# Performance work log

Hardware: AMD Instinct MI355X
Metric: run time of the kernel (lower is better)

Reference implementation:

```python
import jax, jax.numpy as jnp
import numpy as np

N_QUBITS = 10
N_LAYERS = 4
OUTPUT = 16
BATCH = 4096
DIM = 2 ** N_QUBITS  # 1024, amplitude-embedding dimension


def setup_inputs() -> dict:
    key = jax.random.key(0)
    k1, k2, k3, k4 = jax.random.split(key, 4)
    X = jax.random.normal(k1, (BATCH, DIM), jnp.float32)
    weights = jax.random.normal(k2, (N_LAYERS, N_QUBITS, 3), jnp.float32)  # StronglyEntanglingLayers params
    W = jax.random.normal(k3, (OUTPUT, N_QUBITS), jnp.float32) / np.sqrt(N_QUBITS)
    b = jax.random.normal(k4, (OUTPUT,), jnp.float32) * 0.01
    return {"X": X, "weights": weights, "W": W, "b": b}


def _rot_matrix(phi, theta, omega):
    # PennyLane Rot(phi, theta, omega) = RZ(omega) @ RY(theta) @ RZ(phi)
    c = jnp.cos(theta / 2).astype(jnp.complex64)
    s = jnp.sin(theta / 2).astype(jnp.complex64)
    a = jnp.exp(-0.5j * (phi + omega)) * c
    bq = -jnp.exp(0.5j * (phi - omega)) * s
    cq = jnp.exp(-0.5j * (phi - omega)) * s
    d = jnp.exp(0.5j * (phi + omega)) * c
    return jnp.stack([jnp.stack([a, bq]), jnp.stack([cq, d])])  # (2,2) complex64


def _apply_1q(state, U, q, n):
    # wire 0 is the most-significant bit (PennyLane default.qubit convention)
    A, B = 2 ** q, 2 ** (n - q - 1)
    s = state.reshape(-1, A, 2, B)
    s = jnp.einsum('ij,bajc->baic', U, s)
    return s.reshape(-1, 2 ** n)


def _cnot(state, c, t, n):
    hi, lo = (c, t) if c < t else (t, c)
    s = state.reshape(-1, 2 ** hi, 2, 2 ** (lo - hi - 1), 2, 2 ** (n - lo - 1))
    if c < t:
        # control axis 2, target axis 4
        s0 = s[:, :, 0]                      # (B, H, M, 2, L)
        s1 = jnp.flip(s[:, :, 1], axis=3)    # flip target where control=1
        s = jnp.stack([s0, s1], axis=2)
    else:
        # control axis 4, target axis 2
        s0 = s[:, :, :, :, 0, :]             # (B, H, 2, M, L)
        s1 = jnp.flip(s[:, :, :, :, 1, :], axis=2)
        s = jnp.stack([s0, s1], axis=4)
    return s.reshape(-1, 2 ** n)


def _circuit(X, weights):
    n = N_QUBITS
    # AmplitudeEmbedding (pad_with=0.0; here input dim == 2**n so just normalize)
    nrm = jnp.linalg.norm(X, axis=-1, keepdims=True)
    state = (X / nrm).astype(jnp.complex64)  # (B, 2**n)
    for l in range(N_LAYERS):
        for q in range(n):
            U = _rot_matrix(weights[l, q, 0], weights[l, q, 1], weights[l, q, 2])
            state = _apply_1q(state, U, q, n)
        r = (l % (n - 1)) + 1  # StronglyEntanglingLayers default imprimitive range
        for q in range(n):
            state = _cnot(state, q, (q + r) % n, n)
    probs = state.real ** 2 + state.imag ** 2  # (B, 2**n)
    # <Z_i> = sum_s probs[s] * (1 - 2*bit_i(s)); wire 0 = MSB
    idx = np.arange(2 ** n)
    bits = (idx[:, None] >> np.arange(n - 1, -1, -1)[None, :]) & 1  # (2**n, n)
    signs = jnp.asarray(1 - 2 * bits, jnp.float32)
    return probs @ signs  # (B, n)


def reference(X, weights, W, b):
    z = _circuit(X, weights)          # (B, n_qubits)
    return z @ W.T + b                # Linear head; nn.Tanh is defined but unused in forward
```

## Files before the change

kernel.cpp:

```cpp
#include <hip/hip_runtime.h>
#include <stdint.h>

#define NQ 10
#define DIMQ 1024
#define BATCH 4096

typedef float f32x2 __attribute__((ext_vector_type(2)));

#if __has_builtin(__builtin_amdgcn_permlane16_swap)
#define HAS_PL16 1
#else
#define HAS_PL16 0
#endif

__host__ __device__ constexpr int cperm_c(int x, int r) {
  for (int q = 0; q < NQ; ++q) {
    const int c = 9 - q;
    int t = c - r; if (t < 0) t += NQ;
    x ^= ((x >> c) & 1) << t;
  }
  return x;
}
constexpr int amask(int q) {
  int a = 0;
  for (int b = 0; b < 6; ++b) a |= ((cperm_c(1 << b, 4) >> (9 - q)) & 1) << b;
  return a;
}
constexpr int mmask(int q) {
  int m = 0;
  for (int b = 0; b < 4; ++b) m |= ((cperm_c(1 << (6 + b), 4) >> (9 - q)) & 1) << b;
  return m;
}

__global__ __launch_bounds__(256) void prep_g(const float* __restrict__ wts,
                                              float* __restrict__ Gg) {
  const int idx = blockIdx.x * 256 + threadIdx.x;
  if (idx < 40) {
    float th = wts[idx * 3 + 1];
    ((float2*)Gg)[idx] = make_float2(cosf(0.5f * th), sinf(0.5f * th));
  }
  f32x2* D0 = (f32x2*)(Gg + 128);
  float4* E = (float4*)(D0 + 1024);
  auto sphase = [&](int l, int i, int comp) {
    float s = 0.f;
    #pragma unroll
    for (int q = 0; q < 10; ++q) {
      float sg = ((i >> (9 - q)) & 1) ? 0.5f : -0.5f;
      s += sg * wts[(l * 10 + q) * 3 + comp];
    }
    return s;
  };
  float p0 = sphase(0, idx, 0);
  D0[idx] = (f32x2){cosf(p0), sinf(p0)};
  #pragma unroll
  for (int l = 0; l < 3; ++l) {
    float a = sphase(l, idx, 2) + sphase(l + 1, cperm_c(idx, l + 1), 0);
    E[l * 1024 + idx] = make_float4(cosf(a), cosf(a), -sinf(a), sinf(a));
  }
}

template<int CTRL>
__device__ __forceinline__ float dpp1(float x) {
  return __int_as_float(
      __builtin_amdgcn_update_dpp(0, __float_as_int(x), CTRL, 0xF, 0xF, true));
}
template<int P>
__device__ __forceinline__ float shufl(float x) {
  if constexpr (P == 0)      return dpp1<0xB1>(x);
  else if constexpr (P == 1) return dpp1<0x4E>(x);
  else if constexpr (P == 2) return dpp1<0x141>(dpp1<0x1B>(x));
  else                       return dpp1<0x128>(x);
}

__device__ __forceinline__ f32x2 swapv(f32x2 v) {
  return __builtin_shufflevector(v, v, 1, 0);
}

__device__ __forceinline__ float red64(float v) {
  v += dpp1<0xB1>(v);
  v += dpp1<0x4E>(v);
  v += dpp1<0x141>(dpp1<0x1B>(v));
  v += dpp1<0x128>(v);
#if HAS_PL16
  { auto rr = __builtin_amdgcn_permlane16_swap(__float_as_uint(v),
                                               __float_as_uint(v), false, false);
    v = __uint_as_float(rr[0]) + __uint_as_float(rr[1]); }
#else
  v += __int_as_float(__builtin_amdgcn_ds_swizzle(__float_as_int(v), 0x401F));
#endif
  auto p = __builtin_amdgcn_permlane32_swap(__float_as_uint(v),
                                            __float_as_uint(v), false, false);
  return __uint_as_float(p[0]) + __uint_as_float(p[1]);
}

template<int MT>
__device__ __forceinline__ void ry_reg(f32x2 (&s)[16], float2 cs) {
  const float c = cs.x, sn = cs.y;
  #pragma unroll
  for (int e0 = 0; e0 < 16; ++e0) {
    if (e0 & MT) continue;
    const int e1 = e0 | MT;
    f32x2 x0 = s[e0], x1 = s[e1];
    s[e0] = c * x0 - sn * x1;
    s[e1] = sn * x0 + c * x1;
  }
}
template<int P>
__device__ __forceinline__ void ry_dpp(f32x2 (&s)[16], float2 cs, int lane) {
  const float c = cs.x;
  const float ss = ((lane >> P) & 1) ? cs.y : -cs.y;
  #pragma unroll
  for (int e = 0; e < 16; ++e) {
    f32x2 o;
    o.x = shufl<P>(s[e].x);
    o.y = shufl<P>(s[e].y);
    s[e] = c * s[e] + ss * o;
  }
}
__device__ __forceinline__ void ry16(f32x2 (&s)[16], float2 cs, int lane) {
  const bool H = (lane & 16) != 0;
#if HAS_PL16
  const float b0 = H ? cs.y : 0.f;
  const float b1 = H ? 0.f : -cs.y;
  const float c = cs.x;
  #pragma unroll
  for (int e = 0; e < 16; ++e) {
    auto rr = __builtin_amdgcn_permlane16_swap(__float_as_uint(s[e].x),
                                               __float_as_uint(s[e].x), false, false);
    auto ri = __builtin_amdgcn_permlane16_swap(__float_as_uint(s[e].y),
                                               __float_as_uint(s[e].y), false, false);
    f32x2 o0, o1;
    o0.x = __uint_as_float(rr[0]); o0.y = __uint_as_float(ri[0]);
    o1.x = __uint_as_float(rr[1]); o1.y = __uint_as_float(ri[1]);
    s[e] = c * s[e] + b0 * o0 + b1 * o1;
  }
#else
  const float c = cs.x;
  const float ss = H ? cs.y : -cs.y;
  #pragma unroll
  for (int e = 0; e < 16; ++e) {
    f32x2 o;
    o.x = __int_as_float(__builtin_amdgcn_ds_swizzle(__float_as_int(s[e].x), 0x401F));
    o.y = __int_as_float(__builtin_amdgcn_ds_swizzle(__float_as_int(s[e].y), 0x401F));
    s[e] = c * s[e] + ss * o;
  }
#endif
}
__device__ __forceinline__ void ry5(f32x2 (&s)[16], float2 cs, int lane) {
  const int L = lane >> 5;
  const float c = cs.x;
  const float a0 = L ? cs.y : 0.f;
  const float a1 = L ? 0.f : -cs.y;
  #pragma unroll
  for (int e = 0; e < 16; ++e) {
    auto rr = __builtin_amdgcn_permlane32_swap(__float_as_uint(s[e].x),
                                               __float_as_uint(s[e].x), false, false);
    auto ri = __builtin_amdgcn_permlane32_swap(__float_as_uint(s[e].y),
                                               __float_as_uint(s[e].y), false, false);
    f32x2 o0, o1;
    o0.x = __uint_as_float(rr[0]); o0.y = __uint_as_float(ri[0]);
    o1.x = __uint_as_float(rr[1]); o1.y = __uint_as_float(ri[1]);
    s[e] = c * s[e] + a0 * o0 + a1 * o1;
  }
}

template<int R>
__device__ __forceinline__ void perm_state(f32x2 (&s)[16], f32x2* __restrict__ L,
                                           int lane) {
  constexpr int K0=cperm_c(1,R),  K1=cperm_c(2,R),  K2=cperm_c(4,R),
                K3=cperm_c(8,R),  K4=cperm_c(16,R), K5=cperm_c(32,R),
                C6=cperm_c(64,R), C7=cperm_c(128,R),
                C8=cperm_c(256,R),C9=cperm_c(512,R);
  const int yl = ((lane & 1)  ? K0 : 0) ^ ((lane & 2)  ? K1 : 0) ^
                 ((lane & 4)  ? K2 : 0) ^ ((lane & 8)  ? K3 : 0) ^
                 ((lane & 16) ? K4 : 0) ^ ((lane & 32) ? K5 : 0);
  #pragma unroll
  for (int e = 0; e < 16; ++e) {
    const int ye = ((e & 1) ? C6 : 0) ^ ((e & 2) ? C7 : 0) ^
                   ((e & 4) ? C8 : 0) ^ ((e & 8) ? C9 : 0);
    L[yl ^ ye] = s[e];
  }
  #pragma unroll
  for (int e = 0; e < 16; ++e) s[e] = L[(e << 6) | lane];
}

template<int LYR>
__device__ __forceinline__ void do_layer(f32x2 (&s)[16],
                                         const float2* __restrict__ ryc,
                                         const float4* __restrict__ Etab,
                                         f32x2* __restrict__ L, int lane) {
  float4 et[16];
  if constexpr (LYR < 3) {
    const float4* El = Etab + LYR * 1024;
    #pragma unroll
    for (int e = 0; e < 16; ++e) et[e] = El[(e << 6) | lane];
  }
  const float2* G = ryc + LYR * 10;
  ry_reg<8>(s, G[0]);
  ry_reg<4>(s, G[1]);
  ry_reg<2>(s, G[2]);
  ry_reg<1>(s, G[3]);
  ry5     (s, G[4], lane);
  ry16    (s, G[5], lane);
  ry_dpp<3>(s, G[6], lane);
  ry_dpp<2>(s, G[7], lane);
  ry_dpp<1>(s, G[8], lane);
  ry_dpp<0>(s, G[9], lane);
  if constexpr (LYR < 3) {
    #pragma unroll
    for (int e = 0; e < 16; ++e) {
      f32x2 e1; e1.x = et[e].x; e1.y = et[e].y;
      f32x2 e2; e2.x = et[e].z; e2.y = et[e].w;
      s[e] = e1 * s[e] + e2 * swapv(s[e]);
    }
    perm_state<LYR + 1>(s, L, lane);
  }
}

template<int M>
__device__ __forceinline__ void wht(float (&h)[16]) {
  #pragma unroll
  for (int e0 = 0; e0 < 16; ++e0) {
    if (e0 & M) continue;
    float u = h[e0], v = h[e0 | M];
    h[e0] = u + v;
    h[e0 | M] = u - v;
  }
}
template<int Q>
__device__ __forceinline__ float zfin(const float (&h)[16], int lane) {
  constexpr int aq = amask(Q);
  constexpr int mq = mmask(Q);
  float t = h[mq];
  if constexpr (aq != 0) {
    int par = __builtin_popcount(lane & aq) & 1;
    t = par ? -t : t;
  }
  return red64(t);
}

__global__ __launch_bounds__(256, 2) void vqc_sim(const float* __restrict__ X,
                                                  const float* __restrict__ Gg,
                                                  const float* __restrict__ W,
                                                  const float* __restrict__ bias,
                                                  float* __restrict__ out) {
  __shared__ f32x2 lds[4][DIMQ];
  const int lane = threadIdx.x & 63;
  const int w = threadIdx.x >> 6;
  const int row = blockIdx.x * 4 + w;
  f32x2* L = lds[w];
  const float2* ryc = (const float2*)Gg;
  const f32x2* D0   = (const f32x2*)(Gg + 128);
  const float4* Etab = (const float4*)(D0 + 1024);

  f32x2 s[16];

  const float* xr = X + (size_t)row * DIMQ;
  float ss = 0.f;
  #pragma unroll
  for (int e = 0; e < 16; ++e) {
    float v = xr[(e << 6) | lane];
    ss += v * v;
    s[e] = v * D0[(e << 6) | lane];
  }
  const float rn2 = 1.0f / red64(ss);

  do_layer<0>(s, ryc, Etab, L, lane);
  do_layer<1>(s, ryc, Etab, L, lane);
  do_layer<2>(s, ryc, Etab, L, lane);
  do_layer<3>(s, ryc, Etab, L, lane);

  float h[16];
  #pragma unroll
  for (int e = 0; e < 16; ++e) h[e] = s[e].x * s[e].x + s[e].y * s[e].y;
  wht<1>(h); wht<2>(h); wht<4>(h); wht<8>(h);

  float z[10];
  z[0] = zfin<0>(h, lane);
  z[1] = zfin<1>(h, lane);
  z[2] = zfin<2>(h, lane);
  z[3] = zfin<3>(h, lane);
  z[4] = zfin<4>(h, lane);
  z[5] = zfin<5>(h, lane);
  z[6] = zfin<6>(h, lane);
  z[7] = zfin<7>(h, lane);
  z[8] = zfin<8>(h, lane);
  z[9] = zfin<9>(h, lane);

  if (lane < 16) {
    float acc = 0.f;
    #pragma unroll
    for (int q = 0; q < 10; ++q) acc += z[q] * W[lane * 10 + q];
    out[(size_t)row * 16 + lane] = bias[lane] + rn2 * acc;
  }
}

extern "C" void kernel_launch(void* const* d_in, const int* in_sizes, int n_in,
                              void* d_out, int out_size, void* d_ws, size_t ws_size,
                              hipStream_t stream) {
  const float* X    = (const float*)d_in[0];
  const float* wts  = (const float*)d_in[1];
  const float* W    = (const float*)d_in[2];
  const float* bias = (const float*)d_in[3];
  float* out = (float*)d_out;
  float* Gg = (float*)d_ws;

  hipLaunchKernelGGL(prep_g,  dim3(4),         dim3(256), 0, stream, wts, Gg);
  hipLaunchKernelGGL(vqc_sim, dim3(BATCH / 4), dim3(256), 0, stream, X, Gg, W, bias, out);
}
```

Baseline: 97.51 us.

## Use three-shear rotations for in-register RY and ds_swizzle for lane-xor-4 exchange

After: 94.63 us. 1.03x faster.

```diff
diff --git a/kernel.cpp b/kernel.cpp
--- a/kernel.cpp
+++ b/kernel.cpp
@@ -37,9 +37,10 @@
   const int idx = blockIdx.x * 256 + threadIdx.x;
   if (idx < 40) {
     float th = wts[idx * 3 + 1];
-    ((float2*)Gg)[idx] = make_float2(cosf(0.5f * th), sinf(0.5f * th));
-  }
-  f32x2* D0 = (f32x2*)(Gg + 128);
+    ((float4*)Gg)[idx] = make_float4(cosf(0.5f * th), sinf(0.5f * th),
+                                     tanf(0.25f * th), 0.f);
+  }
+  f32x2* D0 = (f32x2*)(Gg + 256);
   float4* E = (float4*)(D0 + 1024);
   auto sphase = [&](int l, int i, int comp) {
     float s = 0.f;
@@ -68,7 +69,6 @@
 __device__ __forceinline__ float shufl(float x) {
   if constexpr (P == 0)      return dpp1<0xB1>(x);
   else if constexpr (P == 1) return dpp1<0x4E>(x);
-  else if constexpr (P == 2) return dpp1<0x141>(dpp1<0x1B>(x));
   else                       return dpp1<0x128>(x);
 }
 
@@ -94,15 +94,14 @@
 }
 
 template<int MT>
-__device__ __forceinline__ void ry_reg(f32x2 (&s)[16], float2 cs) {
-  const float c = cs.x, sn = cs.y;
+__device__ __forceinline__ void ry_reg(f32x2 (&s)[16], float t, float sn) {
   #pragma unroll
   for (int e0 = 0; e0 < 16; ++e0) {
     if (e0 & MT) continue;
     const int e1 = e0 | MT;
-    f32x2 x0 = s[e0], x1 = s[e1];
-    s[e0] = c * x0 - sn * x1;
-    s[e1] = sn * x0 + c * x1;
+    s[e0] = s[e0] - t * s[e1];
+    s[e1] = s[e1] + sn * s[e0];
+    s[e0] = s[e0] - t * s[e1];
   }
 }
 template<int P>
@@ -114,6 +113,17 @@
     f32x2 o;
     o.x = shufl<P>(s[e].x);
     o.y = shufl<P>(s[e].y);
+    s[e] = c * s[e] + ss * o;
+  }
+}
+__device__ __forceinline__ void ry_ds4(f32x2 (&s)[16], float2 cs, int lane) {
+  const float c = cs.x;
+  const float ss = ((lane >> 2) & 1) ? cs.y : -cs.y;
+  #pragma unroll
+  for (int e = 0; e < 16; ++e) {
+    f32x2 o;
+    o.x = __int_as_float(__builtin_amdgcn_ds_swizzle(__float_as_int(s[e].x), 0x101F));
+    o.y = __int_as_float(__builtin_amdgcn_ds_swizzle(__float_as_int(s[e].y), 0x101F));
     s[e] = c * s[e] + ss * o;
   }
 }
@@ -186,7 +196,7 @@
 
 template<int LYR>
 __device__ __forceinline__ void do_layer(f32x2 (&s)[16],
-                                         const float2* __restrict__ ryc,
+                                         const float4* __restrict__ gq,
                                          const float4* __restrict__ Etab,
                                          f32x2* __restrict__ L, int lane) {
   float4 et[16];
@@ -195,17 +205,17 @@
     #pragma unroll
     for (int e = 0; e < 16; ++e) et[e] = El[(e << 6) | lane];
   }
-  const float2* G = ryc + LYR * 10;
-  ry_reg<8>(s, G[0]);
-  ry_reg<4>(s, G[1]);
-  ry_reg<2>(s, G[2]);
-  ry_reg<1>(s, G[3]);
-  ry5     (s, G[4], lane);
-  ry16    (s, G[5], lane);
-  ry_dpp<3>(s, G[6], lane);
-  ry_dpp<2>(s, G[7], lane);
-  ry_dpp<1>(s, G[8], lane);
-  ry_dpp<0>(s, G[9], lane);
+  const float4* G = gq + LYR * 10;
+  ry_reg<8>(s, G[0].z, G[0].y);
+  ry_reg<4>(s, G[1].z, G[1].y);
+  ry_reg<2>(s, G[2].z, G[2].y);
+  ry_reg<1>(s, G[3].z, G[3].y);
+  ry5     (s, make_float2(G[4].x, G[4].y), lane);
+  ry16    (s, make_float2(G[5].x, G[5].y), lane);
+  ry_dpp<3>(s, make_float2(G[6].x, G[6].y), lane);
+  ry_ds4  (s, make_float2(G[7].x, G[7].y), lane);
+  ry_dpp<1>(s, make_float2(G[8].x, G[8].y), lane);
+  ry_dpp<0>(s, make_float2(G[9].x, G[9].y), lane);
   if constexpr (LYR < 3) {
     #pragma unroll
     for (int e = 0; e < 16; ++e) {
@@ -249,8 +259,8 @@
   const int w = threadIdx.x >> 6;
   const int row = blockIdx.x * 4 + w;
   f32x2* L = lds[w];
-  const float2* ryc = (const float2*)Gg;
-  const f32x2* D0   = (const f32x2*)(Gg + 128);
+  const float4* gq  = (const float4*)Gg;
+  const f32x2* D0   = (const f32x2*)(Gg + 256);
   const float4* Etab = (const float4*)(D0 + 1024);
 
   f32x2 s[16];
@@ -265,10 +275,10 @@
   }
   const float rn2 = 1.0f / red64(ss);
 
-  do_layer<0>(s, ryc, Etab, L, lane);
-  do_layer<1>(s, ryc, Etab, L, lane);
-  do_layer<2>(s, ryc, Etab, L, lane);
-  do_layer<3>(s, ryc, Etab, L, lane);
+  do_layer<0>(s, gq, Etab, L, lane);
+  do_layer<1>(s, gq, Etab, L, lane);
+  do_layer<2>(s, gq, Etab, L, lane);
+  do_layer<3>(s, gq, Etab, L, lane);
 
   float h[16];
   #pragma unroll
```
